# Performance work log

Measured on AMD Instinct MI355X. Metric: run time of the kernel, lower is better.

The kernel has to match this reference:

```python
import jax, jax.numpy as jnp
from jax import lax
import numpy as np

L, B, C, H, W = 2, 4, 256, 128, 128
D = C // 2            # complex feature dim per head (embed_dim // 2)
NH = 2                # hardcoded n_heads in ComplexTransformerEncoderLayer
KS, STRIDE, PAD = 9, 8, 4
SCALE = 32.0 ** -0.5  # n_head_channels ** -0.5 (hardcoded 32)

_PNAMES = ['wq','bq','wk','bk','wv','bv','off_dw_w','off_dw_b','off_ln_g','off_ln_b',
           'off_pw_w','fc1_wr','fc1_wi','fc1_br','fc1_bi','fc2_wr','fc2_wi','fc2_br',
           'fc2_bi','ln_grr','ln_gri','ln_gii','ln_br','ln_bi','rpe_table']


def _bilinear(img, grid):
    # img: (Cc, Hi, Wi); grid: (..., 2) with (x, y) in [-1, 1]
    # matches F.grid_sample(mode='bilinear', align_corners=True, padding_mode='zeros')
    Cc, Hi, Wi = img.shape
    x = (grid[..., 0] + 1.0) * 0.5 * (Wi - 1)
    y = (grid[..., 1] + 1.0) * 0.5 * (Hi - 1)
    x0 = jnp.floor(x); y0 = jnp.floor(y)
    x1 = x0 + 1.0; y1 = y0 + 1.0
    wx1 = x - x0; wx0 = 1.0 - wx1
    wy1 = y - y0; wy0 = 1.0 - wy1

    def tap(yy, xx, wgt):
        valid = (xx >= 0) & (xx <= Wi - 1) & (yy >= 0) & (yy <= Hi - 1)
        xi = jnp.clip(xx, 0, Wi - 1).astype(jnp.int32)
        yi = jnp.clip(yy, 0, Hi - 1).astype(jnp.int32)
        v = img[:, yi, xi]                      # (Cc, *grid_shape)
        return v * (wgt * valid.astype(img.dtype))[None]

    return (tap(y0, x0, wy0 * wx0) + tap(y0, x1, wy0 * wx1)
            + tap(y1, x0, wy1 * wx0) + tap(y1, x1, wy1 * wx1))

_grid_sample = jax.vmap(_bilinear)


def _cln(a, b, gam, eps=1e-20):
    # complex layer-norm via 2x2 covariance whitening over the last (feature) dim
    grr, gri, gii, br, bi = gam
    a = a - a.mean(-1, keepdims=True)
    b = b - b.mean(-1, keepdims=True)
    vrr = (a * a).mean(-1, keepdims=True) + eps
    vii = (b * b).mean(-1, keepdims=True) + eps
    vri = (a * b).mean(-1, keepdims=True)
    s = jnp.sqrt(vrr * vii - vri * vri)
    t = jnp.sqrt(vrr + vii + 2.0 * s)
    inv = 1.0 / (s * t)
    wrr = (vii + s) * inv; wii = (vrr + s) * inv; wri = -vri * inv
    na = wrr * a + wri * b
    nb = wri * a + wii * b
    return grr * na + gri * nb + br, gri * na + gii * nb + bi


def _layer(xa, xb, p):
    res_a = xa.reshape(B * NH, D, H * W).transpose(2, 0, 1)  # (HW, B*NH, D)
    res_b = xb.reshape(B * NH, D, H * W).transpose(2, 0, 1)

    def proj(x, w, bias):  # 1x1 conv
        return jnp.einsum('bchw,oc->bohw', x, w) + bias[None, :, None, None]

    qa = proj(xa, p['wq'], p['bq'])
    qb = proj(xb, p['wq'], p['bq'])

    def conv_offset(q):
        y = lax.conv_general_dilated(q, p['off_dw_w'], (STRIDE, STRIDE),
                                     ((PAD, PAD), (PAD, PAD)),
                                     feature_group_count=C,
                                     dimension_numbers=('NCHW', 'OIHW', 'NCHW'))
        y = y + p['off_dw_b'][None, :, None, None]
        m = y.mean(1, keepdims=True)
        v = ((y - m) ** 2).mean(1, keepdims=True)
        y = (y - m) * lax.rsqrt(v + 1e-5)
        y = y * p['off_ln_g'][None, :, None, None] + p['off_ln_b'][None, :, None, None]
        y = jax.nn.gelu(y, approximate=False)
        return jnp.einsum('bchw,pc->bhwp', y, p['off_pw_w'])  # (B, Hk, Wk, 2) in (y, x)

    off_a = conv_offset(qa)
    off_b = conv_offset(qb)
    Hk, Wk = off_a.shape[1], off_a.shape[2]
    ns = Hk * Wk

    ry = jnp.linspace(0.5, Hk - 0.5, Hk) / (Hk - 1.0) * 2.0 - 1.0
    rx = jnp.linspace(0.5, Wk - 0.5, Wk) / (Wk - 1.0) * 2.0 - 1.0
    ref = jnp.stack(jnp.meshgrid(ry, rx, indexing='ij'), -1)  # (Hk, Wk, 2) (y, x)
    pos_a = off_a + ref
    pos_b = off_b + ref

    xs_a = _grid_sample(xa, pos_a[..., ::-1])  # (B, C, Hk, Wk)
    xs_b = _grid_sample(xb, pos_b[..., ::-1])

    ka = proj(xs_a, p['wk'], p['bk']).reshape(B * NH, D, ns)
    va = proj(xs_a, p['wv'], p['bv']).reshape(B * NH, D, ns)
    kb = proj(xs_b, p['wk'], p['bk']).reshape(B * NH, D, ns)
    vb = proj(xs_b, p['wv'], p['bv']).reshape(B * NH, D, ns)
    qa_ = qa.reshape(B * NH, D, H * W)
    qb_ = qb.reshape(B * NH, D, H * W)

    # Re( q * conj(k) ); imaginary part is discarded by attn.real in the original
    attn = SCALE * (jnp.einsum('bcm,bcn->bmn', qa_, ka)
                    + jnp.einsum('bcm,bcn->bmn', qb_, kb))

    # deformable RPE bias; only the real (a) branch survives attn.real
    gy = jnp.arange(H, dtype=xa.dtype) / (H - 1.0) * 2.0 - 1.0
    gx = jnp.arange(W, dtype=xa.dtype) / (W - 1.0) * 2.0 - 1.0
    qg = jnp.stack(jnp.meshgrid(gy, gx, indexing='ij'), -1).reshape(H * W, 2)
    disp_a = (qg[None, :, None, :] - pos_a.reshape(B, ns, 2)[:, None, :, :]) * 0.5
    rpe = jnp.broadcast_to(p['rpe_table'][None], (B, NH, 2 * H - 1, 2 * W - 1))
    bias_a = _grid_sample(rpe, disp_a[..., ::-1]).reshape(B * NH, H * W, ns)

    attn = jax.nn.softmax(attn + bias_a, axis=2)
    oa = jnp.einsum('bmn,bcn->bcm', attn, va).transpose(2, 0, 1)  # (HW, B*NH, D)
    ob = jnp.einsum('bmn,bcn->bcm', attn, vb).transpose(2, 0, 1)

    oa, ob = _cln(oa, ob, (p['ln_grr'][0], p['ln_gri'][0], p['ln_gii'][0],
                           p['ln_br'][0], p['ln_bi'][0]))
    xa2 = res_a + oa
    xb2 = res_b + ob

    def clinear(a, b, wr, wi, br, bi):
        ya = a @ wr.T - b @ wi.T + br
        yb = a @ wi.T + b @ wr.T + bi
        return ya, yb

    ha, hb = clinear(xa2, xb2, p['fc1_wr'], p['fc1_wi'], p['fc1_br'], p['fc1_bi'])
    ha = jax.nn.relu(ha); hb = jax.nn.relu(hb)
    ha, hb = clinear(ha, hb, p['fc2_wr'], p['fc2_wi'], p['fc2_br'], p['fc2_bi'])
    ha, hb = _cln(ha, hb, (p['ln_grr'][1], p['ln_gri'][1], p['ln_gii'][1],
                           p['ln_br'][1], p['ln_bi'][1]))
    xa3 = xa2 + ha
    xb3 = xb2 + hb
    return (xa3.transpose(1, 2, 0).reshape(B, C, H, W),
            xb3.transpose(1, 2, 0).reshape(B, C, H, W))


def _forward(x_A, x_B, stacked):
    for l in range(L):
        p = {n: stacked[n][l] for n in _PNAMES}
        x_A, x_B = _layer(x_A, x_B, p)
    return x_A, x_B


def setup_inputs():
    key = jax.random.key(0)
    ks = jax.random.split(key, 12)
    f32 = jnp.float32
    return {
        'x_A': jax.random.normal(ks[0], (B, C, H, W), f32),
        'x_B': jax.random.normal(ks[1], (B, C, H, W), f32),
        'wq': jax.random.normal(ks[2], (L, C, C), f32) / np.float32(np.sqrt(C)),
        'bq': jnp.zeros((L, C), f32),
        'wk': jax.random.normal(ks[3], (L, C, C), f32) / np.float32(np.sqrt(C)),
        'bk': jnp.zeros((L, C), f32),
        'wv': jax.random.normal(ks[4], (L, C, C), f32) / np.float32(np.sqrt(C)),
        'bv': jnp.zeros((L, C), f32),
        'off_dw_w': jax.random.normal(ks[5], (L, C, 1, KS, KS), f32) * 0.05,
        'off_dw_b': jnp.zeros((L, C), f32),
        'off_ln_g': jnp.ones((L, C), f32),
        'off_ln_b': jnp.zeros((L, C), f32),
        'off_pw_w': jax.random.normal(ks[6], (L, 2, C), f32) * 0.01,
        'fc1_wr': jax.random.normal(ks[7], (L, D, D), f32) / np.float32(np.sqrt(D)),
        'fc1_wi': jax.random.normal(ks[8], (L, D, D), f32) / np.float32(np.sqrt(D)),
        'fc1_br': jnp.zeros((L, D), f32),
        'fc1_bi': jnp.zeros((L, D), f32),
        'fc2_wr': jax.random.normal(ks[9], (L, D, D), f32) / np.float32(np.sqrt(D)),
        'fc2_wi': jax.random.normal(ks[10], (L, D, D), f32) / np.float32(np.sqrt(D)),
        'fc2_br': jnp.zeros((L, D), f32),
        'fc2_bi': jnp.zeros((L, D), f32),
        'ln_grr': jnp.full((L, 2, D), 1.0 / np.sqrt(2.0), f32),
        'ln_gri': jnp.zeros((L, 2, D), f32),
        'ln_gii': jnp.full((L, 2, D), 1.0 / np.sqrt(2.0), f32),
        'ln_br': jnp.zeros((L, 2, D), f32),
        'ln_bi': jnp.zeros((L, 2, D), f32),
        # original forward creates rpe_table as fresh zeros each call
        'rpe_table': jnp.zeros((L, NH, 2 * H - 1, 2 * W - 1), f32),
    }


def reference(x_A, x_B, wq, bq, wk, bk, wv, bv, off_dw_w, off_dw_b, off_ln_g, off_ln_b,
              off_pw_w, fc1_wr, fc1_wi, fc1_br, fc1_bi, fc2_wr, fc2_wi, fc2_br, fc2_bi,
              ln_grr, ln_gri, ln_gii, ln_br, ln_bi, rpe_table):
    vals = (wq, bq, wk, bk, wv, bv, off_dw_w, off_dw_b, off_ln_g, off_ln_b, off_pw_w,
            fc1_wr, fc1_wi, fc1_br, fc1_bi, fc2_wr, fc2_wi, fc2_br, fc2_bi,
            ln_grr, ln_gri, ln_gii, ln_br, ln_bi, rpe_table)
    stacked = {n: v for n, v in zip(_PNAMES, vals)}
    return _forward(x_A, x_B, stacked)
```

## Files before the change

kernel.cpp:

```cpp
#include <hip/hip_runtime.h>
#include <math.h>

#define DEVFN static __device__ __forceinline__

constexpr int LAYERS = 2;
constexpr int Bz = 4;
constexpr int Cc = 256;
constexpr int Hh = 128;
constexpr int Ww = 128;
constexpr int Dd = 128;
constexpr int NHh = 2;
constexpr int BHt = Bz * NHh;
constexpr int Mt  = Hh * Ww;
constexpr int HK = 16, WK = 16;
constexpr int NSs = HK * WK;
constexpr int STR = 8, PADc = 4;
constexpr int RPH = 2*Hh - 1, RPW = 2*Ww - 1;
constexpr float SCALE_F = 0.17677669529663687f;

typedef __attribute__((ext_vector_type(8))) short  bf16x8;
typedef __attribute__((ext_vector_type(4))) float  f32x4;

DEVFN float wsum64(float v) {
    #pragma unroll
    for (int off = 32; off > 0; off >>= 1) v += __shfl_xor(v, off, 64);
    return v;
}

DEVFN void split2(float x, ushort& h, ushort& l)
{
    const uint u  = __float_as_uint(x);
    const uint hb = (u + 0x7fffu + ((u >> 16) & 1u)) & 0xffff0000u;
    h = (ushort)(hb >> 16);
    const float r = x - __uint_as_float(hb);
    const uint ul = __float_as_uint(r);
    l = (ushort)((ul + 0x7fffu + ((ul >> 16) & 1u)) >> 16);
}

DEVFN ushort f2bf(float x)
{
    const uint u = __float_as_uint(x);
    return (ushort)((u + 0x7fffu + ((u >> 16) & 1u)) >> 16);
}
DEVFN float bf2f(ushort s) { return __uint_as_float(((uint)s) << 16); }

DEVFN uint shfu(uint v, int src) { return (uint)__shfl((int)v, src, 64); }

DEVFN bf16x8 pack4(uint a, uint b, uint c, uint d)
{
    union { uint u[4]; bf16x8 v; } t;
    t.u[0] = a; t.u[1] = b; t.u[2] = c; t.u[3] = d;
    return t.v;
}

DEVFN void unpack8(uint4 a, uint4 b, bf16x8& h, bf16x8& l)
{
    const uint u[8] = {a.x, a.y, a.z, a.w, b.x, b.y, b.z, b.w};
    #pragma unroll
    for (int j = 0; j < 8; j++) {
        h[j] = (short)(u[j] >> 16);
        l[j] = (short)(u[j] & 0xffffu);
    }
}

__global__ __launch_bounds__(256)
void k_proj(const float* __restrict__ X, const float* __restrict__ W,
            const float* __restrict__ bias, float* __restrict__ Out, int Mdim)
{
    __shared__ float wsm[16][64];
    __shared__ float xsm[16][64];
    const int tid = threadIdx.x;
    const int m0 = blockIdx.x * 64;
    const int o0 = blockIdx.y * 64;
    const float* Xb = X + (size_t)blockIdx.z * Cc * Mdim;
    float* Ob = Out + (size_t)blockIdx.z * Cc * Mdim;
    const int to = tid >> 4;
    const int tm = tid & 15;
    float acc[4][4] = {{0.f}};
    for (int k0 = 0; k0 < Cc; k0 += 16) {
        {
            const int i = tid >> 2, kq = tid & 3;
            float4 w4 = *(const float4*)(W + (size_t)(o0 + i)*Cc + k0 + kq*4);
            wsm[kq*4+0][i] = w4.x; wsm[kq*4+1][i] = w4.y;
            wsm[kq*4+2][i] = w4.z; wsm[kq*4+3][i] = w4.w;
            const int kk = tid >> 4, jq = tid & 15;
            *(float4*)&xsm[kk][jq*4] =
                *(const float4*)(Xb + (size_t)(k0 + kk)*Mdim + m0 + jq*4);
        }
        __syncthreads();
        #pragma unroll
        for (int kk = 0; kk < 16; kk++) {
            float4 a4 = *(const float4*)&wsm[kk][to*4];
            float4 b4 = *(const float4*)&xsm[kk][tm*4];
            float av[4] = {a4.x, a4.y, a4.z, a4.w};
            float bv[4] = {b4.x, b4.y, b4.z, b4.w};
            #pragma unroll
            for (int ii = 0; ii < 4; ii++)
                #pragma unroll
                for (int jj = 0; jj < 4; jj++)
                    acc[ii][jj] += av[ii] * bv[jj];
        }
        __syncthreads();
    }
    #pragma unroll
    for (int ii = 0; ii < 4; ii++) {
        const int o = o0 + to*4 + ii;
        const float bo = bias[o];
        float4 r4 = make_float4(acc[ii][0]+bo, acc[ii][1]+bo, acc[ii][2]+bo, acc[ii][3]+bo);
        *(float4*)(Ob + (size_t)o*Mdim + m0 + tm*4) = r4;
    }
}

__global__ __launch_bounds__(256)
void k_projq_mfma(const uint* __restrict__ Xt, const uint* __restrict__ Wqp,
                  const float* __restrict__ bias, float* __restrict__ Out,
                  int s)
{
    __shared__ __align__(16) float ot[256 * 68];
    const int tid = threadIdx.x;
    const int m0 = blockIdx.x * 64;
    const int b  = blockIdx.y;
    const int w = tid >> 6, l = tid & 63;
    const int l15 = l & 15, g = l >> 4;
    const int m = m0 + w*16 + l15;

    bf16x8 xh[8], xl[8];
    {
        const uint* xp0 = Xt + ((size_t)(b*2 + 0)*Mt + m)*256 + s*128 + g*8;
        const uint* xp1 = Xt + ((size_t)(b*2 + 1)*Mt + m)*256 + s*128 + g*8;
        #pragma unroll
        for (int cs = 0; cs < 8; cs++) {
            const uint* xp = ((cs < 4) ? xp0 : xp1) + (cs & 3)*32;
            const uint4 x0 = *(const uint4*)(xp);
            const uint4 x1 = *(const uint4*)(xp + 4);
            unpack8(x0, x1, xh[cs], xl[cs]);
        }
    }

    f32x4 acc[16];
    #pragma unroll
    for (int nt = 0; nt < 16; nt++) acc[nt] = (f32x4){0.f, 0.f, 0.f, 0.f};

    const uint* wp = Wqp + l15*256 + g*8;
    #pragma unroll
    for (int cs = 0; cs < 8; cs++) {
        #pragma unroll
        for (int nt = 0; nt < 16; nt++) {
            const uint* wpp = wp + nt*4096 + cs*32;
            const uint4 w0 = *(const uint4*)(wpp);
            const uint4 w1 = *(const uint4*)(wpp + 4);
            bf16x8 wh, wl; unpack8(w0, w1, wh, wl);
            acc[nt] = __builtin_amdgcn_mfma_f32_16x16x32_bf16(wh, xh[cs], acc[nt], 0, 0, 0);
            acc[nt] = __builtin_amdgcn_mfma_f32_16x16x32_bf16(wh, xl[cs], acc[nt], 0, 0, 0);
            acc[nt] = __builtin_amdgcn_mfma_f32_16x16x32_bf16(wl, xh[cs], acc[nt], 0, 0, 0);
        }
    }

    #pragma unroll
    for (int nt = 0; nt < 16; nt++) {
        #pragma unroll
        for (int r = 0; r < 4; r++) {
            const int o = nt*16 + g*4 + r;
            ot[o*68 + w*16 + l15] = acc[nt][r] + bias[o];
        }
    }
    __syncthreads();
    #pragma unroll
    for (int it = 0; it < 16; it++) {
        const int idx = it*256 + tid;
        const int o = idx >> 4, mq = idx & 15;
        const float4 v = *(const float4*)&ot[o*68 + mq*4];
        *(float4*)(Out + ((size_t)b*Cc + o)*Mt + m0 + mq*4) = v;
    }
}

__global__ __launch_bounds__(256)
void k_dwconv(const float* __restrict__ Q, const float* __restrict__ Wdw,
              const float* __restrict__ Bdw, float* __restrict__ Y)
{
    const int c = blockIdx.x, b = blockIdx.y;
    __shared__ float wsmem[81];
    const int tid = threadIdx.x;
    if (tid < 81) wsmem[tid] = Wdw[c*81 + tid];
    __syncthreads();
    const int i = tid >> 4, j = tid & 15;
    const float* Qc = Q + ((size_t)b*Cc + c)*Mt;
    float acc = Bdw[c];
    const int ybase = i*STR - PADc, xbase = j*STR - PADc;
    #pragma unroll
    for (int u = 0; u < 9; u++) {
        const int y = ybase + u;
        if (y < 0 || y >= Hh) continue;
        #pragma unroll
        for (int v = 0; v < 9; v++) {
            const int x = xbase + v;
            if (x < 0 || x >= Ww) continue;
            acc += wsmem[u*9+v] * Qc[y*Ww + x];
        }
    }
    Y[((size_t)b*Cc + c)*NSs + i*WK + j] = acc;
}

DEVFN float block_reduce(float v, float* red, int tid)
{
    red[tid] = v; __syncthreads();
    #pragma unroll
    for (int s2 = 128; s2 > 0; s2 >>= 1) {
        if (tid < s2) red[tid] += red[tid + s2];
        __syncthreads();
    }
    const float r = red[0];
    __syncthreads();
    return r;
}

__global__ __launch_bounds__(256)
void k_lnpw(const float* __restrict__ Y, const float* __restrict__ G,
            const float* __restrict__ Bt, const float* __restrict__ PW,
            float* __restrict__ Pos)
{
    __shared__ float red[256];
    const int ij = blockIdx.x, b = blockIdx.y;
    const int tid = threadIdx.x;
    const float y = Y[((size_t)b*Cc + tid)*NSs + ij];
    const float m = block_reduce(y, red, tid) * (1.f/256.f);
    const float d = y - m;
    const float v = block_reduce(d*d, red, tid) * (1.f/256.f);
    const float g = d * rsqrtf(v + 1e-5f) * G[tid] + Bt[tid];
    const float ge = 0.5f * g * (1.f + erff(g * 0.70710678118654752f));
    const float off0 = block_reduce(ge * PW[tid], red, tid);
    const float off1 = block_reduce(ge * PW[Cc + tid], red, tid);
    if (tid == 0) {
        const int i = ij >> 4, j = ij & 15;
        const float refy = ((float)i + 0.5f) * (2.f/15.f) - 1.f;
        const float refx = ((float)j + 0.5f) * (2.f/15.f) - 1.f;
        Pos[((size_t)b*NSs + ij)*2 + 0] = off0 + refy;
        Pos[((size_t)b*NSs + ij)*2 + 1] = off1 + refx;
    }
}

__global__ __launch_bounds__(256)
void k_gsample(const float* __restrict__ X, const float* __restrict__ Pos,
               float* __restrict__ Xs)
{
    const int c = blockIdx.x, b = blockIdx.y, s = threadIdx.x;
    const float py = Pos[((size_t)b*NSs + s)*2 + 0];
    const float px = Pos[((size_t)b*NSs + s)*2 + 1];
    const float x = (px + 1.f) * 0.5f * (float)(Ww - 1);
    const float y = (py + 1.f) * 0.5f * (float)(Hh - 1);
    const float x0 = floorf(x), y0 = floorf(y);
    const float wx1 = x - x0, wx0 = 1.f - wx1;
    const float wy1 = y - y0, wy0 = 1.f - wy1;
    const float* Xc = X + ((size_t)b*Cc + c)*Mt;
    float acc = 0.f;
    #pragma unroll
    for (int t = 0; t < 4; t++) {
        const float xx = x0 + (float)(t & 1);
        const float yy = y0 + (float)(t >> 1);
        float w = ((t & 1) ? wx1 : wx0) * ((t >> 1) ? wy1 : wy0);
        const bool valid = (xx >= 0.f) && (xx <= (float)(Ww-1)) &&
                           (yy >= 0.f) && (yy <= (float)(Hh-1));
        const int xi = (int)fminf(fmaxf(xx, 0.f), (float)(Ww-1));
        const int yi = (int)fminf(fmaxf(yy, 0.f), (float)(Hh-1));
        acc += (valid ? w : 0.f) * Xc[yi*Ww + xi];
    }
    Xs[((size_t)b*Cc + c)*NSs + s] = acc;
}

__global__ __launch_bounds__(256)
void k_qsplit(const float* __restrict__ Qa, const float* __restrict__ Qb,
              uint* __restrict__ Qs)
{
    __shared__ float tile[64][65];
    const int tid = threadIdx.x;
    const int m0 = blockIdx.x * 64;
    const int bh = blockIdx.y;
    const int b = bh >> 1, h = bh & 1;
    for (int ccblk = 0; ccblk < 4; ccblk++) {
        #pragma unroll
        for (int i = 0; i < 4; i++) {
            const int idx = i*256 + tid;
            const int ccl = idx >> 4, mq = idx & 15;
            const int cc2 = ccblk*64 + ccl;
            const float* src = (cc2 >> 7) ? Qb : Qa;
            *(float4*)&tile[ccl][mq*4] =
                *(const float4*)(src + ((size_t)b*Cc + h*Dd + (cc2 & 127))*Mt + m0 + mq*4);
        }
        __syncthreads();
        #pragma unroll
        for (int i = 0; i < 16; i++) {
            const int idx = i*256 + tid;
            const int ml = idx >> 6, ccl = idx & 63;
            ushort hi, lo; split2(tile[ccl][ml], hi, lo);
            Qs[((size_t)bh*Mt + m0 + ml)*256 + ccblk*64 + ccl] = ((uint)hi << 16) | lo;
        }
        __syncthreads();
    }
}

__global__ __launch_bounds__(256)
void k_ksplit(const float* __restrict__ Ka, const float* __restrict__ Kb,
              uint* __restrict__ Ktp)
{
    __shared__ float tile[64][65];
    const int tid = threadIdx.x;
    const int n0 = blockIdx.x * 64;
    const int bh = blockIdx.y;
    const int b = bh >> 1, h = bh & 1;
    for (int ccblk = 0; ccblk < 4; ccblk++) {
        #pragma unroll
        for (int i = 0; i < 16; i++) {
            const int idx = i*256 + tid;
            const int ccl = idx >> 6, nl = idx & 63;
            const int cc2 = ccblk*64 + ccl;
            const float* src = (cc2 >> 7) ? Kb : Ka;
            tile[ccl][nl] = src[((size_t)b*Cc + h*Dd + (cc2 & 127))*NSs + n0 + nl];
        }
        __syncthreads();
        #pragma unroll
        for (int i = 0; i < 16; i++) {
            const int idx = i*256 + tid;
            const int nl = idx >> 6, ccl = idx & 63;
            ushort hi, lo; split2(tile[ccl][nl], hi, lo);
            Ktp[((size_t)bh*NSs + n0 + nl)*256 + ccblk*64 + ccl] = ((uint)hi << 16) | lo;
        }
        __syncthreads();
    }
}

__global__ __launch_bounds__(256)
void k_vsplit(const float* __restrict__ Va, const float* __restrict__ Vb,
              uint* __restrict__ Vsp)
{
    const size_t e = (size_t)blockIdx.x*256 + threadIdx.x;
    const int n  = (int)(e & 255);
    const int j  = (int)((e >> 8) & 255);
    const int bh = (int)(e >> 16);
    const int b = bh >> 1, h = bh & 1;
    const float* src = (j >> 7) ? Vb : Va;
    const float v = src[((size_t)b*Cc + h*Dd + (j & 127))*NSs + n];
    ushort hi, lo; split2(v, hi, lo);
    Vsp[e] = ((uint)hi << 16) | lo;
}

__global__ __launch_bounds__(256)
void k_wsplit4(const float* __restrict__ W0, const float* __restrict__ W1,
               const float* __restrict__ W2, const float* __restrict__ W3,
               uint* __restrict__ Wp)
{
    const int mat = blockIdx.y;
    const float* W = (mat == 0) ? W0 : (mat == 1) ? W1 : (mat == 2) ? W2 : W3;
    const int i = blockIdx.x*256 + threadIdx.x;
    ushort hi, lo; split2(W[i], hi, lo);
    Wp[(size_t)mat*Dd*Dd + i] = ((uint)hi << 16) | lo;
}

__global__ __launch_bounds__(256)
void k_wsplit1(const float* __restrict__ W, uint* __restrict__ Wp)
{
    const int i = blockIdx.x*256 + threadIdx.x;
    ushort hi, lo; split2(W[i], hi, lo);
    Wp[i] = ((uint)hi << 16) | lo;
}

__global__ __launch_bounds__(256, 2)
void k_attn_mfma(const uint* __restrict__ Qs, const uint* __restrict__ Ktp,
                 const uint* __restrict__ Vsp,
                 const float* __restrict__ Pos, const float* __restrict__ Rpe,
                 float* __restrict__ Oa, float* __restrict__ Ob)
{
    constexpr int GS = 66;
    __shared__ ushort Gt[NSs * GS];
    __shared__ float fxs[NSs];
    __shared__ __align__(16) uint kvbuf[2][4096];
    const int tid = threadIdx.x;
    const int m0 = blockIdx.x * 64;
    const int bh = blockIdx.y;
    const int b = bh >> 1, h = bh & 1;
    const int j0 = m0 & 127;
    const int iq = m0 >> 7;
    const float* Rh = Rpe + (size_t)h * RPH * RPW;

    {
        const int n = tid;
        const float py = Pos[((size_t)b*NSs + n)*2 + 0];
        const float px = Pos[((size_t)b*NSs + n)*2 + 1];
        const float xf = (float)j0 + 63.5f - 63.5f*px;
        const float yf = (float)iq + 63.5f - 63.5f*py;
        const float xbf = floorf(xf), ybf = floorf(yf);
        const float fx = xf - xbf, fy = yf - ybf;
        fxs[n] = fx;
        const int yb = (int)ybf;
        const float wy0 = (1.f - fy) * ((yb   >= 0 && yb   <= RPH-1) ? 1.f : 0.f);
        const float wy1 = fy         * ((yb+1 >= 0 && yb+1 <= RPH-1) ? 1.f : 0.f);
        const int y0c = yb   < 0 ? 0 : (yb   > RPH-1 ? RPH-1 : yb);
        const int y1c = yb+1 < 0 ? 0 : (yb+1 > RPH-1 ? RPH-1 : yb+1);
        const float* r0 = Rh + (size_t)y0c * RPW;
        const float* r1 = Rh + (size_t)y1c * RPW;
        const int xb = (int)xbf;
        #pragma unroll 4
        for (int t = 0; t <= 64; t++) {
            const int xi = xb + t;
            const int xc = xi < 0 ? 0 : (xi > RPW-1 ? RPW-1 : xi);
            const float v = wy0*r0[xc] + wy1*r1[xc];
            Gt[n*GS + t] = f2bf((xi >= 0 && xi <= RPW-1) ? v : 0.f);
        }
    }

    const int w = tid >> 6, l = tid & 63;
    const int l15 = l & 15, g = l >> 4;
    const int mcol = m0 + w*16 + l15;

    const uint* kbase = Ktp + (size_t)bh * 65536;
    const uint* vbase = Vsp + (size_t)bh * 65536;
    char* const kv0 = (char*)&kvbuf[0][0];
    char* const kv1 = (char*)&kvbuf[1][0];
    auto stage = [&](int p, const uint* chunk) {
        char* dst = p ? kv1 : kv0;
        #pragma unroll
        for (int r = 0; r < 4; r++) {
            const int idx = r*1024 + tid*4;
            const uint4 v = *(const uint4*)(chunk + idx);
            const int byte = idx << 2;
            const int swz = ((byte >> 10) & 7) << 4;
            *(uint4*)(dst + (byte ^ swz)) = v;
        }
    };

    bf16x8 qh[8], ql[8];
    {
        const uint* qp = Qs + ((size_t)bh*Mt + mcol)*256 + g*8;
        #pragma unroll
        for (int cs = 0; cs < 8; cs++) {
            const uint4 q0 = *(const uint4*)(qp + cs*32);
            const uint4 q1 = *(const uint4*)(qp + cs*32 + 4);
            unpack8(q0, q1, qh[cs], ql[cs]);
        }
    }

    f32x4 acc[16];
    #pragma unroll
    for (int nt = 0; nt < 16; nt++) acc[nt] = (f32x4){0.f, 0.f, 0.f, 0.f};

    const int rowb = l15 << 10;
    const int sw = (l15 & 7) << 4;

    stage(0, kbase);
    __syncthreads();
    #pragma unroll
    for (int nt = 0; nt < 16; nt++) {
        if (nt < 15) stage((nt + 1) & 1, kbase + (nt + 1)*4096);
        const char* bufc = (nt & 1) ? kv1 : kv0;
        #pragma unroll
        for (int cs = 0; cs < 8; cs++) {
            const int a0 = rowb + cs*128 + g*32;
            const uint4 k0 = *(const uint4*)(bufc + (a0 ^ sw));
            const uint4 k1 = *(const uint4*)(bufc + ((a0 + 16) ^ sw));
            bf16x8 kh, kl; unpack8(k0, k1, kh, kl);
            acc[nt] = __builtin_amdgcn_mfma_f32_16x16x32_bf16(kh, qh[cs], acc[nt], 0, 0, 0);
            acc[nt] = __builtin_amdgcn_mfma_f32_16x16x32_bf16(kh, ql[cs], acc[nt], 0, 0, 0);
            acc[nt] = __builtin_amdgcn_mfma_f32_16x16x32_bf16(kl, qh[cs], acc[nt], 0, 0, 0);
        }
        __syncthreads();
    }

    const int dm = w*16 + l15;
    float mx = -1e30f;
    #pragma unroll
    for (int nt = 0; nt < 16; nt++) {
        #pragma unroll
        for (int r = 0; r < 4; r++) {
            const int n = nt*16 + g*4 + r;
            const float g0 = bf2f(Gt[n*GS + dm]);
            const float g1 = bf2f(Gt[n*GS + dm + 1]);
            const float bias = g0 + fxs[n]*(g1 - g0);
            const float s = SCALE_F*acc[nt][r] + bias;
            acc[nt][r] = s;
            mx = fmaxf(mx, s);
        }
    }
    mx = fmaxf(mx, __shfl_xor(mx, 16, 64));
    mx = fmaxf(mx, __shfl_xor(mx, 32, 64));
    float sum = 0.f;
    #pragma unroll
    for (int nt = 0; nt < 16; nt++)
        #pragma unroll
        for (int r = 0; r < 4; r++) {
            const float e = __expf(acc[nt][r] - mx);
            acc[nt][r] = e;
            sum += e;
        }
    sum += __shfl_xor(sum, 16, 64);
    sum += __shfl_xor(sum, 32, 64);
    const float inv = 1.f / sum;

    uint hU0[16], hU1[16], lU0[16], lU1[16];
    #pragma unroll
    for (int nt = 0; nt < 16; nt++) {
        ushort ph_[4], pl_[4];
        #pragma unroll
        for (int r = 0; r < 4; r++) split2(acc[nt][r] * inv, ph_[r], pl_[r]);
        hU0[nt] = (uint)ph_[0] | ((uint)ph_[1] << 16);
        hU1[nt] = (uint)ph_[2] | ((uint)ph_[3] << 16);
        lU0[nt] = (uint)pl_[0] | ((uint)pl_[1] << 16);
        lU1[nt] = (uint)pl_[2] | ((uint)pl_[3] << 16);
    }

    const int srcA = (((2*g)     & 3) << 4) | l15;
    const int srcB = (((2*g + 1) & 3) << 4) | l15;
    const bool hi2 = (g >> 1) & 1;
    bf16x8 ph[8], pl[8];
    #pragma unroll
    for (int cs = 0; cs < 8; cs++) {
        uint A00 = shfu(hU0[2*cs], srcA), A01 = shfu(hU0[2*cs+1], srcA);
        uint A10 = shfu(hU1[2*cs], srcA), A11 = shfu(hU1[2*cs+1], srcA);
        uint B00 = shfu(hU0[2*cs], srcB), B01 = shfu(hU0[2*cs+1], srcB);
        uint B10 = shfu(hU1[2*cs], srcB), B11 = shfu(hU1[2*cs+1], srcB);
        ph[cs] = pack4(hi2 ? A01 : A00, hi2 ? A11 : A10,
                       hi2 ? B01 : B00, hi2 ? B11 : B10);
        A00 = shfu(lU0[2*cs], srcA); A01 = shfu(lU0[2*cs+1], srcA);
        A10 = shfu(lU1[2*cs], srcA); A11 = shfu(lU1[2*cs+1], srcA);
        B00 = shfu(lU0[2*cs], srcB); B01 = shfu(lU0[2*cs+1], srcB);
        B10 = shfu(lU1[2*cs], srcB); B11 = shfu(lU1[2*cs+1], srcB);
        pl[cs] = pack4(hi2 ? A01 : A00, hi2 ? A11 : A10,
                       hi2 ? B01 : B00, hi2 ? B11 : B10);
    }

    const size_t rowbase = ((size_t)bh*Mt + mcol)*Dd;
    stage(0, vbase);
    __syncthreads();
    for (int jt = 0; jt < 16; jt++) {
        if (jt < 15) stage((jt + 1) & 1, vbase + (jt + 1)*4096);
        const char* bufc = (jt & 1) ? kv1 : kv0;
        f32x4 a2 = (f32x4){0.f, 0.f, 0.f, 0.f};
        #pragma unroll
        for (int cs = 0; cs < 8; cs++) {
            const int a0 = rowb + cs*128 + g*32;
            const uint4 v0 = *(const uint4*)(bufc + (a0 ^ sw));
            const uint4 v1 = *(const uint4*)(bufc + ((a0 + 16) ^ sw));
            bf16x8 vh, vl; unpack8(v0, v1, vh, vl);
            a2 = __builtin_amdgcn_mfma_f32_16x16x32_bf16(vh, ph[cs], a2, 0, 0, 0);
            a2 = __builtin_amdgcn_mfma_f32_16x16x32_bf16(vh, pl[cs], a2, 0, 0, 0);
            a2 = __builtin_amdgcn_mfma_f32_16x16x32_bf16(vl, ph[cs], a2, 0, 0, 0);
        }
        const float4 o = make_float4(a2[0], a2[1], a2[2], a2[3]);
        const int jv0 = jt*16 + g*4;
        if (jt < 8) *(float4*)(Oa + rowbase + jv0) = o;
        else        *(float4*)(Ob + rowbase + jv0 - 128) = o;
        __syncthreads();
    }
}

__global__ __launch_bounds__(256)
void k_cln_attn(const float* __restrict__ Oa, const float* __restrict__ Ob,
                const float* __restrict__ Xa, const float* __restrict__ Xb,
                const float* __restrict__ Pgrr, const float* __restrict__ Pgri,
                const float* __restrict__ Pgii, const float* __restrict__ Pbr,
                const float* __restrict__ Pbi,
                float* __restrict__ X2a, float* __restrict__ X2b)
{
    __shared__ float ra[32][132];
    __shared__ float rb[32][132];
    const int tid = threadIdx.x;
    const int m0 = blockIdx.x * 32;
    const int bh = blockIdx.y;
    const int b = bh >> 1, h = bh & 1;
    {
        const float* Xpa = Xa + ((size_t)b*Cc + h*Dd)*Mt + m0;
        const float* Xpb = Xb + ((size_t)b*Cc + h*Dd)*Mt + m0;
        for (int idx = tid; idx < 1024; idx += 256) {
            const int c = idx >> 3, jq = idx & 7;
            float4 a4 = *(const float4*)(Xpa + (size_t)c*Mt + jq*4);
            float4 b4 = *(const float4*)(Xpb + (size_t)c*Mt + jq*4);
            ra[jq*4+0][c] = a4.x; ra[jq*4+1][c] = a4.y;
            ra[jq*4+2][c] = a4.z; ra[jq*4+3][c] = a4.w;
            rb[jq*4+0][c] = b4.x; rb[jq*4+1][c] = b4.y;
            rb[jq*4+2][c] = b4.z; rb[jq*4+3][c] = b4.w;
        }
    }
    __syncthreads();
    const int wave = tid >> 6, lane = tid & 63;
    const float grr0 = Pgrr[lane], grr1 = Pgrr[lane+64];
    const float gri0 = Pgri[lane], gri1 = Pgri[lane+64];
    const float gii0 = Pgii[lane], gii1 = Pgii[lane+64];
    const float br0  = Pbr[lane],  br1  = Pbr[lane+64];
    const float bi0  = Pbi[lane],  bi1  = Pbi[lane+64];
    for (int r = wave; r < 32; r += 4) {
        const size_t rowoff = ((size_t)bh*Mt + m0 + r)*Dd;
        float a0 = Oa[rowoff + lane], a1 = Oa[rowoff + lane + 64];
        float c0 = Ob[rowoff + lane], c1 = Ob[rowoff + lane + 64];
        const float ma = wsum64(a0 + a1) * (1.f/128.f);
        const float mb = wsum64(c0 + c1) * (1.f/128.f);
        a0 -= ma; a1 -= ma; c0 -= mb; c1 -= mb;
        const float vrr = wsum64(a0*a0 + a1*a1) * (1.f/128.f) + 1e-20f;
        const float vii = wsum64(c0*c0 + c1*c1) * (1.f/128.f) + 1e-20f;
        const float vri = wsum64(a0*c0 + a1*c1) * (1.f/128.f);
        const float s = sqrtf(fmaxf(vrr*vii - vri*vri, 0.f));
        const float t = sqrtf(vrr + vii + 2.f*s);
        const float inv = 1.f / (s*t);
        const float wrr = (vii + s)*inv, wii = (vrr + s)*inv, wri = -vri*inv;
        const float na0 = wrr*a0 + wri*c0, nb0 = wri*a0 + wii*c0;
        const float na1 = wrr*a1 + wri*c1, nb1 = wri*a1 + wii*c1;
        X2a[rowoff + lane]      = ra[r][lane]    + grr0*na0 + gri0*nb0 + br0;
        X2a[rowoff + lane + 64] = ra[r][lane+64] + grr1*na1 + gri1*nb1 + br1;
        X2b[rowoff + lane]      = rb[r][lane]    + gri0*na0 + gii0*nb0 + bi0;
        X2b[rowoff + lane + 64] = rb[r][lane+64] + gri1*na1 + gii1*nb1 + bi1;
    }
}

__global__ __launch_bounds__(256)
void k_ffn_mfma(const float* __restrict__ A, const float* __restrict__ Bm,
                const uint* __restrict__ Wrp, const uint* __restrict__ Wip,
                const float* __restrict__ br, const float* __restrict__ bi,
                float* __restrict__ Ha, float* __restrict__ Hb, int relu)
{
    const int tid = threadIdx.x;
    const size_t r0 = (size_t)blockIdx.x * 64;
    const int w = tid >> 6, l = tid & 63;
    const int l15 = l & 15, g = l >> 4;
    const size_t row = r0 + (size_t)w*16 + l15;

    f32x4 accr[8], acci[8];
    #pragma unroll
    for (int nt = 0; nt < 8; nt++) {
        accr[nt] = (f32x4){0.f, 0.f, 0.f, 0.f};
        acci[nt] = (f32x4){0.f, 0.f, 0.f, 0.f};
    }

    const float* ap = A  + row*Dd + g*8;
    const float* bp = Bm + row*Dd + g*8;
    const uint*  wr = Wrp + l15*Dd + g*8;
    const uint*  wi = Wip + l15*Dd + g*8;

    #pragma unroll
    for (int cs = 0; cs < 4; cs++) {
        const float4 a0 = *(const float4*)(ap + cs*32);
        const float4 a1 = *(const float4*)(ap + cs*32 + 4);
        const float4 b0 = *(const float4*)(bp + cs*32);
        const float4 b1 = *(const float4*)(bp + cs*32 + 4);
        const float av[8] = {a0.x,a0.y,a0.z,a0.w,a1.x,a1.y,a1.z,a1.w};
        const float bv[8] = {b0.x,b0.y,b0.z,b0.w,b1.x,b1.y,b1.z,b1.w};
        bf16x8 ah, al, bh_, bl_, nh, nl;
        #pragma unroll
        for (int j = 0; j < 8; j++) {
            ushort h1, l1; split2(av[j], h1, l1);
            ah[j] = (short)h1; al[j] = (short)l1;
            split2(bv[j], h1, l1);
            bh_[j] = (short)h1; bl_[j] = (short)l1;
            nh[j] = (short)(h1 ^ 0x8000);
            nl[j] = (short)(l1 ^ 0x8000);
        }
        #pragma unroll
        for (int nt = 0; nt < 8; nt++) {
            const uint* wrp2 = wr + nt*2048 + cs*32;
            const uint* wip2 = wi + nt*2048 + cs*32;
            const uint4 r0v = *(const uint4*)(wrp2);
            const uint4 r1v = *(const uint4*)(wrp2 + 4);
            const uint4 i0v = *(const uint4*)(wip2);
            const uint4 i1v = *(const uint4*)(wip2 + 4);
            bf16x8 wrh, wrl, wih, wil;
            unpack8(r0v, r1v, wrh, wrl);
            unpack8(i0v, i1v, wih, wil);
            accr[nt] = __builtin_amdgcn_mfma_f32_16x16x32_bf16(wrh, ah, accr[nt], 0, 0, 0);
            accr[nt] = __builtin_amdgcn_mfma_f32_16x16x32_bf16(wrh, al, accr[nt], 0, 0, 0);
            accr[nt] = __builtin_amdgcn_mfma_f32_16x16x32_bf16(wrl, ah, accr[nt], 0, 0, 0);
            accr[nt] = __builtin_amdgcn_mfma_f32_16x16x32_bf16(wih, nh, accr[nt], 0, 0, 0);
            accr[nt] = __builtin_amdgcn_mfma_f32_16x16x32_bf16(wih, nl, accr[nt], 0, 0, 0);
            accr[nt] = __builtin_amdgcn_mfma_f32_16x16x32_bf16(wil, nh, accr[nt], 0, 0, 0);
            acci[nt] = __builtin_amdgcn_mfma_f32_16x16x32_bf16(wih, ah, acci[nt], 0, 0, 0);
            acci[nt] = __builtin_amdgcn_mfma_f32_16x16x32_bf16(wih, al, acci[nt], 0, 0, 0);
            acci[nt] = __builtin_amdgcn_mfma_f32_16x16x32_bf16(wil, ah, acci[nt], 0, 0, 0);
            acci[nt] = __builtin_amdgcn_mfma_f32_16x16x32_bf16(wrh, bh_, acci[nt], 0, 0, 0);
            acci[nt] = __builtin_amdgcn_mfma_f32_16x16x32_bf16(wrh, bl_, acci[nt], 0, 0, 0);
            acci[nt] = __builtin_amdgcn_mfma_f32_16x16x32_bf16(wrl, bh_, acci[nt], 0, 0, 0);
        }
    }

    #pragma unroll
    for (int nt = 0; nt < 8; nt++) {
        const int n0 = nt*16 + g*4;
        const float4 vbr = *(const float4*)(br + n0);
        const float4 vbi = *(const float4*)(bi + n0);
        const float brv[4] = {vbr.x, vbr.y, vbr.z, vbr.w};
        const float biv[4] = {vbi.x, vbi.y, vbi.z, vbi.w};
        float4 orv, oiv;
        float* po = &orv.x; float* pj = &oiv.x;
        #pragma unroll
        for (int r = 0; r < 4; r++) {
            float hr = accr[nt][r] + brv[r];
            float hi = acci[nt][r] + biv[r];
            if (relu) { hr = fmaxf(hr, 0.f); hi = fmaxf(hi, 0.f); }
            po[r] = hr; pj[r] = hi;
        }
        *(float4*)(Ha + row*Dd + n0) = orv;
        *(float4*)(Hb + row*Dd + n0) = oiv;
    }
}

__global__ __launch_bounds__(256)
void k_cln_ffn(const float* __restrict__ Ha2, const float* __restrict__ Hb2,
               const float* __restrict__ X2a, const float* __restrict__ X2b,
               const float* __restrict__ Pgrr, const float* __restrict__ Pgri,
               const float* __restrict__ Pgii, const float* __restrict__ Pbr,
               const float* __restrict__ Pbi,
               float* __restrict__ OutA, float* __restrict__ OutB)
{
    __shared__ float oA[128][36];
    __shared__ float oB[128][36];
    const int tid = threadIdx.x;
    const int m0 = blockIdx.x * 32;
    const int bh = blockIdx.y;
    const int b = bh >> 1, h = bh & 1;
    const int wave = tid >> 6, lane = tid & 63;
    const float grr0 = Pgrr[lane], grr1 = Pgrr[lane+64];
    const float gri0 = Pgri[lane], gri1 = Pgri[lane+64];
    const float gii0 = Pgii[lane], gii1 = Pgii[lane+64];
    const float br0  = Pbr[lane],  br1  = Pbr[lane+64];
    const float bi0  = Pbi[lane],  bi1  = Pbi[lane+64];
    for (int r = wave; r < 32; r += 4) {
        const size_t rowoff = ((size_t)bh*Mt + m0 + r)*Dd;
        float a0 = Ha2[rowoff + lane], a1 = Ha2[rowoff + lane + 64];
        float c0 = Hb2[rowoff + lane], c1 = Hb2[rowoff + lane + 64];
        const float ma = wsum64(a0 + a1) * (1.f/128.f);
        const float mb = wsum64(c0 + c1) * (1.f/128.f);
        a0 -= ma; a1 -= ma; c0 -= mb; c1 -= mb;
        const float vrr = wsum64(a0*a0 + a1*a1) * (1.f/128.f) + 1e-20f;
        const float vii = wsum64(c0*c0 + c1*c1) * (1.f/128.f) + 1e-20f;
        const float vri = wsum64(a0*c0 + a1*c1) * (1.f/128.f);
        const float s = sqrtf(fmaxf(vrr*vii - vri*vri, 0.f));
        const float t = sqrtf(vrr + vii + 2.f*s);
        const float inv = 1.f / (s*t);
        const float wrr = (vii + s)*inv, wii = (vrr + s)*inv, wri = -vri*inv;
        const float na0 = wrr*a0 + wri*c0, nb0 = wri*a0 + wii*c0;
        const float na1 = wrr*a1 + wri*c1, nb1 = wri*a1 + wii*c1;
        oA[lane][r]    = X2a[rowoff + lane]      + grr0*na0 + gri0*nb0 + br0;
        oA[lane+64][r] = X2a[rowoff + lane + 64] + grr1*na1 + gri1*nb1 + br1;
        oB[lane][r]    = X2b[rowoff + lane]      + gri0*na0 + gii0*nb0 + bi0;
        oB[lane+64][r] = X2b[rowoff + lane + 64] + gri1*na1 + gii1*nb1 + bi1;
    }
    __syncthreads();
    const size_t obase = ((size_t)b*Cc + h*Dd)*Mt + m0;
    for (int idx = tid; idx < 1024; idx += 256) {
        const int c = idx >> 3, jq = idx & 7;
        *(float4*)(OutA + obase + (size_t)c*Mt + jq*4) = *(const float4*)&oA[c][jq*4];
        *(float4*)(OutB + obase + (size_t)c*Mt + jq*4) = *(const float4*)&oB[c][jq*4];
    }
}

extern "C" void kernel_launch(void* const* d_in, const int* in_sizes, int n_in,
                              void* d_out, int out_size, void* d_ws, size_t ws_size,
                              hipStream_t stream)
{
    const float* xA0 = (const float*)d_in[0];
    const float* xB0 = (const float*)d_in[1];
    const float* wq  = (const float*)d_in[2];
    const float* bq  = (const float*)d_in[3];
    const float* wk  = (const float*)d_in[4];
    const float* bk  = (const float*)d_in[5];
    const float* wv  = (const float*)d_in[6];
    const float* bv  = (const float*)d_in[7];
    const float* dww = (const float*)d_in[8];
    const float* dwb = (const float*)d_in[9];
    const float* lng = (const float*)d_in[10];
    const float* lnb = (const float*)d_in[11];
    const float* pw  = (const float*)d_in[12];
    const float* f1wr = (const float*)d_in[13];
    const float* f1wi = (const float*)d_in[14];
    const float* f1br = (const float*)d_in[15];
    const float* f1bi = (const float*)d_in[16];
    const float* f2wr = (const float*)d_in[17];
    const float* f2wi = (const float*)d_in[18];
    const float* f2br = (const float*)d_in[19];
    const float* f2bi = (const float*)d_in[20];
    const float* lgrr = (const float*)d_in[21];
    const float* lgri = (const float*)d_in[22];
    const float* lgii = (const float*)d_in[23];
    const float* lbr  = (const float*)d_in[24];
    const float* lbi  = (const float*)d_in[25];
    const float* rpe  = (const float*)d_in[26];

    float* ws = (float*)d_ws;
    const size_t NB = (size_t)Bz * Cc * Mt;
    const size_t SC = (size_t)Bz * Cc * NSs;
    float* Pa  = ws;        float* Pb  = Pa  + NB;
    float* Ra  = Pb  + NB;  float* Rb  = Ra  + NB;
    float* Ya  = Rb  + NB;  float* Yb  = Ya  + SC;
    float* XsA = Yb  + SC;  float* XsB = XsA + SC;
    float* Kab = XsB + SC;  float* Kbb = Kab + SC;
    float* Vab = Kbb + SC;  float* Vbb = Vab + SC;
    float* Sp0 = Vbb + SC;  float* Sp1 = Sp0 + SC;
    float* PosA = Sp1 + SC; float* PosB = PosA + (size_t)Bz*NSs*2;
    float* Wpf  = PosB + (size_t)Bz*NSs*2;

    uint* Qs  = (uint*)Ra;
    uint* Ktp = (uint*)Sp0;
    uint* Vsp = (uint*)Ya;
    uint* Wp  = (uint*)Wpf;
    uint* Wqp = Wp + (size_t)4*Dd*Dd;

    float* outAf = (float*)d_out;
    float* outBf = outAf + NB;

    for (int l = 0; l < LAYERS; l++) {
        const float* pwq = wq + (size_t)l*Cc*Cc;
        const float* pbq = bq + (size_t)l*Cc;
        const float* pwk = wk + (size_t)l*Cc*Cc;
        const float* pbk = bk + (size_t)l*Cc;
        const float* pwv = wv + (size_t)l*Cc*Cc;
        const float* pbv = bv + (size_t)l*Cc;
        const float* pdww = dww + (size_t)l*Cc*81;
        const float* pdwb = dwb + (size_t)l*Cc;
        const float* plng = lng + (size_t)l*Cc;
        const float* plnb = lnb + (size_t)l*Cc;
        const float* ppw  = pw  + (size_t)l*2*Cc;
        const float* p1wr = f1wr + (size_t)l*Dd*Dd;
        const float* p1wi = f1wi + (size_t)l*Dd*Dd;
        const float* p1br = f1br + (size_t)l*Dd;
        const float* p1bi = f1bi + (size_t)l*Dd;
        const float* p2wr = f2wr + (size_t)l*Dd*Dd;
        const float* p2wi = f2wi + (size_t)l*Dd*Dd;
        const float* p2br = f2br + (size_t)l*Dd;
        const float* p2bi = f2bi + (size_t)l*Dd;
        const float* g0rr = lgrr + (size_t)(l*2+0)*Dd;
        const float* g0ri = lgri + (size_t)(l*2+0)*Dd;
        const float* g0ii = lgii + (size_t)(l*2+0)*Dd;
        const float* g0br = lbr  + (size_t)(l*2+0)*Dd;
        const float* g0bi = lbi  + (size_t)(l*2+0)*Dd;
        const float* g1rr = lgrr + (size_t)(l*2+1)*Dd;
        const float* g1ri = lgri + (size_t)(l*2+1)*Dd;
        const float* g1ii = lgii + (size_t)(l*2+1)*Dd;
        const float* g1br = lbr  + (size_t)(l*2+1)*Dd;
        const float* g1bi = lbi  + (size_t)(l*2+1)*Dd;
        const float* prpe = rpe + (size_t)l*NHh*RPH*RPW;

        const float* inA = l ? outAf : xA0;
        const float* inB = l ? outBf : xB0;

        dim3 gW(64, 4);
        k_wsplit4<<<gW, 256, 0, stream>>>(p1wr, p1wi, p2wr, p2wi, Wp);
        k_wsplit1<<<256, 256, 0, stream>>>(pwq, Wqp);

        dim3 gQs(Mt/64, BHt);
        k_qsplit<<<gQs, 256, 0, stream>>>(inA, inB, Qs);

        dim3 gPQ(Mt/64, Bz);
        k_projq_mfma<<<gPQ, 256, 0, stream>>>(Qs, Wqp, pbq, Pa, 0);
        k_projq_mfma<<<gPQ, 256, 0, stream>>>(Qs, Wqp, pbq, Pb, 1);

        dim3 gD(Cc, Bz);
        k_dwconv<<<gD, 256, 0, stream>>>(Pa, pdww, pdwb, Ya);
        k_dwconv<<<gD, 256, 0, stream>>>(Pb, pdww, pdwb, Yb);

        dim3 gL(NSs, Bz);
        k_lnpw<<<gL, 256, 0, stream>>>(Ya, plng, plnb, ppw, PosA);
        k_lnpw<<<gL, 256, 0, stream>>>(Yb, plng, plnb, ppw, PosB);

        dim3 gS(Cc, Bz);
        k_gsample<<<gS, 256, 0, stream>>>(inA, PosA, XsA);
        k_gsample<<<gS, 256, 0, stream>>>(inB, PosB, XsB);

        dim3 gKV(NSs/64, Cc/64, Bz);
        k_proj<<<gKV, 256, 0, stream>>>(XsA, pwk, pbk, Kab, NSs);
        k_proj<<<gKV, 256, 0, stream>>>(XsB, pwk, pbk, Kbb, NSs);
        k_proj<<<gKV, 256, 0, stream>>>(XsA, pwv, pbv, Vab, NSs);
        k_proj<<<gKV, 256, 0, stream>>>(XsB, pwv, pbv, Vbb, NSs);

        dim3 gKs(NSs/64, BHt);
        k_ksplit<<<gKs, 256, 0, stream>>>(Kab, Kbb, Ktp);
        k_vsplit<<<2048, 256, 0, stream>>>(Vab, Vbb, Vsp);
        k_qsplit<<<gQs, 256, 0, stream>>>(Pa, Pb, Qs);

        dim3 gA(Mt/64, BHt);
        k_attn_mfma<<<gA, 256, 0, stream>>>(Qs, Ktp, Vsp, PosA, prpe, Pa, Pb);

        dim3 gC(Mt/32, BHt);
        k_cln_attn<<<gC, 256, 0, stream>>>(Pa, Pb, inA, inB,
                                           g0rr, g0ri, g0ii, g0br, g0bi, Ra, Rb);

        dim3 gF((unsigned)((size_t)BHt*Mt/64));
        k_ffn_mfma<<<gF, 256, 0, stream>>>(Ra, Rb, Wp, Wp + (size_t)Dd*Dd,
                                           p1br, p1bi, Pa, Pb, 1);
        k_ffn_mfma<<<gF, 256, 0, stream>>>(Pa, Pb, Wp + (size_t)2*Dd*Dd,
                                           Wp + (size_t)3*Dd*Dd,
                                           p2br, p2bi, Pa, Pb, 0);

        k_cln_ffn<<<gC, 256, 0, stream>>>(Pa, Pb, Ra, Rb,
                                          g1rr, g1ri, g1ii, g1br, g1bi, outAf, outBf);
    }
    (void)in_sizes; (void)n_in; (void)out_size; (void)ws_size;
}
```

Before: 2.864 ms.

## Stage projection weights through double-buffered swizzled LDS in Q-proj MFMA kernel

Each weight tile for the Q projection was read by every wave straight from global memory. The kernel now has the whole block cooperatively copy one 16 KB weight chunk per output tile into a double-buffered, XOR-swizzled shared buffer, prefetching the next chunk while computing on the current one. The loop order also changes so that output tiles are the outer loop. Launch bounds now ask for 2 blocks per CU. This cuts redundant global and L2 traffic, but adds a block-wide barrier per tile and may raise register pressure under the new occupancy hint.

```diff
diff --git a/kernel.cpp b/kernel.cpp
--- a/kernel.cpp
+++ b/kernel.cpp
@@ -111,12 +111,15 @@
     }
 }
 
-__global__ __launch_bounds__(256)
+__global__ __launch_bounds__(256, 2)
 void k_projq_mfma(const uint* __restrict__ Xt, const uint* __restrict__ Wqp,
                   const float* __restrict__ bias, float* __restrict__ Out,
                   int s)
 {
-    __shared__ __align__(16) float ot[256 * 68];
+    __shared__ __align__(16) char smem[256 * 68 * 4];
+    char* const kv0 = smem;
+    char* const kv1 = smem + 16384;
+    float* const ot = (float*)smem;
     const int tid = threadIdx.x;
     const int m0 = blockIdx.x * 64;
     const int b  = blockIdx.y;
@@ -124,6 +127,18 @@
     const int l15 = l & 15, g = l >> 4;
     const int m = m0 + w*16 + l15;
 
+    auto stage = [&](int p, const uint* chunk) {
+        char* dst = p ? kv1 : kv0;
+        #pragma unroll
+        for (int r = 0; r < 4; r++) {
+            const int idx = r*1024 + tid*4;
+            const uint4 v = *(const uint4*)(chunk + idx);
+            const int byte = idx << 2;
+            const int swz = ((byte >> 10) & 7) << 4;
+            *(uint4*)(dst + (byte ^ swz)) = v;
+        }
+    };
+
     bf16x8 xh[8], xl[8];
     {
         const uint* xp0 = Xt + ((size_t)(b*2 + 0)*Mt + m)*256 + s*128 + g*8;
@@ -141,19 +156,26 @@
     #pragma unroll
     for (int nt = 0; nt < 16; nt++) acc[nt] = (f32x4){0.f, 0.f, 0.f, 0.f};
 
-    const uint* wp = Wqp + l15*256 + g*8;
-    #pragma unroll
-    for (int cs = 0; cs < 8; cs++) {
-        #pragma unroll
-        for (int nt = 0; nt < 16; nt++) {
-            const uint* wpp = wp + nt*4096 + cs*32;
-            const uint4 w0 = *(const uint4*)(wpp);
-            const uint4 w1 = *(const uint4*)(wpp + 4);
+    const int rowb = l15 << 10;
+    const int sw = (l15 & 7) << 4;
+
+    stage(0, Wqp);
+    __syncthreads();
+    #pragma unroll
+    for (int nt = 0; nt < 16; nt++) {
+        if (nt < 15) stage((nt + 1) & 1, Wqp + (nt + 1)*4096);
+        const char* bufc = (nt & 1) ? kv1 : kv0;
+        #pragma unroll
+        for (int cs = 0; cs < 8; cs++) {
+            const int a0 = rowb + cs*128 + g*32;
+            const uint4 w0 = *(const uint4*)(bufc + (a0 ^ sw));
+            const uint4 w1 = *(const uint4*)(bufc + ((a0 + 16) ^ sw));
             bf16x8 wh, wl; unpack8(w0, w1, wh, wl);
             acc[nt] = __builtin_amdgcn_mfma_f32_16x16x32_bf16(wh, xh[cs], acc[nt], 0, 0, 0);
             acc[nt] = __builtin_amdgcn_mfma_f32_16x16x32_bf16(wh, xl[cs], acc[nt], 0, 0, 0);
             acc[nt] = __builtin_amdgcn_mfma_f32_16x16x32_bf16(wl, xh[cs], acc[nt], 0, 0, 0);
         }
+        __syncthreads();
     }
 
     #pragma unroll
```

Result: faster. 2.558 ms (-10.7%).
